# Kernel tuning notes

Measured on AMD Instinct MI355X. Metric: run time of the kernel, lower is better.

## Reference

```python
import jax, jax.numpy as jnp
import numpy as np

# Shapes: [n_boxes, batch, ch, H, W] as produced by Uncropper in the original module.
N_BOXES, BATCH, CH_KQ, CH_V, H, W = 32, 4, 64, 64, 80, 80


def setup_inputs() -> dict:
    key = jax.random.key(0)
    k1, k2, k3 = jax.random.split(key, 3)
    q_big = jax.random.normal(k1, (N_BOXES, BATCH, CH_KQ, H, W), dtype=jnp.float32)
    k_big = jax.random.normal(k2, (N_BOXES, BATCH, CH_KQ, H, W), dtype=jnp.float32)
    v_big = jax.random.normal(k3, (N_BOXES, BATCH, CH_V, H, W), dtype=jnp.float32)
    return {"q_big": q_big, "k_big": k_big, "v_big": v_big}


def reference(q_big, k_big, v_big):
    # Original loop: for i in range(n_boxes):
    #   w = softmax(sum(q_big[i] * k_big, dim=-3, keepdim=True) / sqrt(ch_kq), dim=-5)
    #   delta_big[i] = sum(w * v_big, dim=-5)
    # Vectorized: attention over the box axis, independent per (batch, h, w) pixel.
    scale = 1.0 / np.sqrt(q_big.shape[2]).astype(np.float32)
    # scores[i, j, b, h, w] = <q_big[i, b, :, h, w], k_big[j, b, :, h, w]>
    scores = jnp.einsum('ibchw,jbchw->ijbhw', q_big, k_big) * scale
    w = jax.nn.softmax(scores, axis=1)  # softmax over source box j (dim=-5 in torch)
    delta_big = jnp.einsum('ijbhw,jbchw->ibchw', w, v_big)
    return delta_big
```

## Files before the change

### kernel.cpp

```cpp
#include <hip/hip_runtime.h>


#define NBOX    32
#define NBATCH  4
#define CH      64
#define HW      6400
#define PIX     16
#define NT      512
#define NTILES  (HW / PIX)
#define NUNITS  (NBATCH * NTILES)

typedef __fp16 f16;
typedef f16   f16x2  __attribute__((ext_vector_type(2)));
typedef f16   f16x8  __attribute__((ext_vector_type(8)));
typedef float f32x16 __attribute__((ext_vector_type(16)));

#define SYNC() do { __builtin_amdgcn_sched_barrier(0); __syncthreads(); \
                    __builtin_amdgcn_sched_barrier(0); } while (0)

__device__ __forceinline__ int swz(int L) {
    return L ^ ((((L >> 9) & 3) | (((L >> 13) & 1) << 2)) << 4);
}
__device__ __forceinline__ int swzO(int L) {
    return L ^ ((((L >> 10) & 7) ^ ((L >> 5) & 7)) << 4);
}

#define ZERO16 {0.f,0.f,0.f,0.f,0.f,0.f,0.f,0.f,0.f,0.f,0.f,0.f,0.f,0.f,0.f,0.f}

__global__ __launch_bounds__(NT, 1)
void box_attn_mfma(const float* __restrict__ q, const float* __restrict__ k,
                   const float* __restrict__ v, float* __restrict__ out) {
    __shared__ char sm[65536];
    char* const KF = sm;
    char* const QF = sm + 32768;
    char* const VF = sm;
    char* const OB = sm + 32768;

    const int t    = threadIdx.x;
    const int lane = t & 63;
    const int w    = t >> 6;
    const int h    = lane >> 5;
    const int bid  = blockIdx.x;
    const int unit = (bid & 7) * (NUNITS / 8) + (bid >> 3);
    const int b    = unit / NTILES;
    const int p0   = (unit % NTILES) * PIX;

    auto load_kq = [&](const float* __restrict__ src, int chalf, float4* r) {
#pragma unroll
        for (int rep = 0; rep < 2; ++rep) {
            int u = rep * NT + t;
            int pxq = u & 3, qq = (u >> 2) & 3, kcL = (u >> 4) & 1, box = (u >> 5) & 31;
            int cb = chalf + kcL * 16 + qq * 4;
            const float* g = src + ((size_t)((box * NBATCH + b) * CH + cb)) * HW + p0 + pxq * 4;
            r[rep * 4 + 0] = *(const float4*)(g);
            r[rep * 4 + 1] = *(const float4*)(g + HW);
            r[rep * 4 + 2] = *(const float4*)(g + 2 * HW);
            r[rep * 4 + 3] = *(const float4*)(g + 3 * HW);
        }
    };
    auto write_kq = [&](char* dst, const float4* r) {
#pragma unroll
        for (int rep = 0; rep < 2; ++rep) {
            int u = rep * NT + t;
            int pxq = u & 3, qq = (u >> 2) & 3, kcL = (u >> 4) & 1, box = (u >> 5) & 31;
            int Lb = kcL * 1024 + (box + 32 * (qq & 1)) * 16 + (qq >> 1) * 8;
            const float* f0 = &r[rep * 4 + 0].x;
            const float* f1 = &r[rep * 4 + 1].x;
            const float* f2 = &r[rep * 4 + 2].x;
            const float* f3 = &r[rep * 4 + 3].x;
#pragma unroll
            for (int pi = 0; pi < 4; ++pi) {
                union { f16x2 hh[2]; uint2 u2; } val;
                val.hh[0] = __builtin_amdgcn_cvt_pkrtz(f0[pi], f1[pi]);
                val.hh[1] = __builtin_amdgcn_cvt_pkrtz(f2[pi], f3[pi]);
                *(uint2*)(dst + swz((pxq * 4 + pi) * 2048 + Lb)) = val.u2;
            }
        }
    };
    auto load_v = [&](int coff, float4* r) {
        const size_t JS = (size_t)NBATCH * CH * HW;
#pragma unroll
        for (int rep = 0; rep < 2; ++rep) {
            int u = rep * NT + t;
            int pxq = u & 3, qq = (u >> 2) & 3, jc = (u >> 4) & 1, cL = (u >> 5) & 31;
            const float* g = v + ((size_t)(((jc * 16 + qq * 4) * NBATCH + b) * CH + coff + cL)) * HW
                               + p0 + pxq * 4;
            r[rep * 4 + 0] = *(const float4*)(g);
            r[rep * 4 + 1] = *(const float4*)(g + JS);
            r[rep * 4 + 2] = *(const float4*)(g + 2 * JS);
            r[rep * 4 + 3] = *(const float4*)(g + 3 * JS);
        }
    };
    auto write_v = [&](const float4* r) {
#pragma unroll
        for (int rep = 0; rep < 2; ++rep) {
            int u = rep * NT + t;
            int pxq = u & 3, qq = (u >> 2) & 3, jc = (u >> 4) & 1, cL = (u >> 5) & 31;
            int Lb = jc * 1024 + (cL + 32 * (qq & 1)) * 16 + (qq >> 1) * 8;
            const float* f0 = &r[rep * 4 + 0].x;
            const float* f1 = &r[rep * 4 + 1].x;
            const float* f2 = &r[rep * 4 + 2].x;
            const float* f3 = &r[rep * 4 + 3].x;
#pragma unroll
            for (int pi = 0; pi < 4; ++pi) {
                union { f16x2 hh[2]; uint2 u2; } val;
                val.hh[0] = __builtin_amdgcn_cvt_pkrtz(f0[pi], f1[pi]);
                val.hh[1] = __builtin_amdgcn_cvt_pkrtz(f2[pi], f3[pi]);
                *(uint2*)(VF + swz((pxq * 4 + pi) * 2048 + Lb)) = val.u2;
            }
        }
    };

    auto smax_pack = [&](const f32x16& s, f16x8& fr0, f16x8& fr1) {
        float p[16];
        float m = s[0];
#pragma unroll
        for (int r = 1; r < 16; ++r) m = fmaxf(m, s[r]);
        m = fmaxf(m, __shfl_xor(m, 32, 64));
        float sum = 0.f;
#pragma unroll
        for (int r = 0; r < 16; ++r) { p[r] = __expf((s[r] - m) * 0.125f); sum += p[r]; }
        sum += __shfl_xor(sum, 32, 64);
        float inv = 1.f / sum;
        union { f16x8 v8; f16x2 hh[4]; } u0, u1;
#pragma unroll
        for (int kk = 0; kk < 4; ++kk) {
            u0.hh[kk] = __builtin_amdgcn_cvt_pkrtz(p[2 * kk] * inv,     p[2 * kk + 1] * inv);
            u1.hh[kk] = __builtin_amdgcn_cvt_pkrtz(p[8 + 2 * kk] * inv, p[9 + 2 * kk] * inv);
        }
        fr0 = u0.v8; fr1 = u1.v8;
    };

    f32x16 sA = ZERO16, sB = ZERO16;
    float4 kr[8], qr[8], kr2[8], qr2[8], vr0[8], vr1[8];

    load_kq(k, 0, kr);   load_kq(q, 0, qr);
    load_kq(k, 32, kr2); load_kq(q, 32, qr2);
    load_v(0, vr0);      load_v(32, vr1);

    write_kq(KF, kr);    write_kq(QF, qr);
    SYNC();

#pragma unroll
    for (int kcL = 0; kcL < 2; ++kcL) {
        int LA = kcL * 1024 + lane * 16;
        f16x8 a0 = *(const f16x8*)(KF + swz(w * 2048 + LA));
        f16x8 b0 = *(const f16x8*)(QF + swz(w * 2048 + LA));
        sA = __builtin_amdgcn_mfma_f32_32x32x16_f16(a0, b0, sA, 0, 0, 0);
        f16x8 a1 = *(const f16x8*)(KF + swz((w + 8) * 2048 + LA));
        f16x8 b1 = *(const f16x8*)(QF + swz((w + 8) * 2048 + LA));
        sB = __builtin_amdgcn_mfma_f32_32x32x16_f16(a1, b1, sB, 0, 0, 0);
    }
    SYNC();
    write_kq(KF, kr2); write_kq(QF, qr2);
    SYNC();
#pragma unroll
    for (int kcL = 0; kcL < 2; ++kcL) {
        int LA = kcL * 1024 + lane * 16;
        f16x8 a0 = *(const f16x8*)(KF + swz(w * 2048 + LA));
        f16x8 b0 = *(const f16x8*)(QF + swz(w * 2048 + LA));
        sA = __builtin_amdgcn_mfma_f32_32x32x16_f16(a0, b0, sA, 0, 0, 0);
        f16x8 a1 = *(const f16x8*)(KF + swz((w + 8) * 2048 + LA));
        f16x8 b1 = *(const f16x8*)(QF + swz((w + 8) * 2048 + LA));
        sB = __builtin_amdgcn_mfma_f32_32x32x16_f16(a1, b1, sB, 0, 0, 0);
    }
    SYNC();

    write_v(vr0);
    f16x8 pA0, pA1, pB0, pB1;
    smax_pack(sA, pA0, pA1);
    smax_pack(sB, pB0, pB1);
    SYNC();

    {
        f32x16 oA = ZERO16, oB = ZERO16;
        {
            int LA = lane * 16;
            f16x8 av0 = *(const f16x8*)(VF + swz(w * 2048 + LA));
            oA = __builtin_amdgcn_mfma_f32_32x32x16_f16(av0, pA0, oA, 0, 0, 0);
            f16x8 av1 = *(const f16x8*)(VF + swz((w + 8) * 2048 + LA));
            oB = __builtin_amdgcn_mfma_f32_32x32x16_f16(av1, pB0, oB, 0, 0, 0);
        }
        {
            int LA = 1024 + lane * 16;
            f16x8 av0 = *(const f16x8*)(VF + swz(w * 2048 + LA));
            oA = __builtin_amdgcn_mfma_f32_32x32x16_f16(av0, pA1, oA, 0, 0, 0);
            f16x8 av1 = *(const f16x8*)(VF + swz((w + 8) * 2048 + LA));
            oB = __builtin_amdgcn_mfma_f32_32x32x16_f16(av1, pB1, oB, 0, 0, 0);
        }
        const int i = lane & 31;
#pragma unroll
        for (int r = 0; r < 16; ++r) {
            int cL = (r & 3) + 8 * (r >> 2) + 4 * h;
            *(f16*)(OB + swzO(i * 1024 + cL * 32 + w * 2))       = (f16)oA[r];
            *(f16*)(OB + swzO(i * 1024 + cL * 32 + (w + 8) * 2)) = (f16)oB[r];
        }
        SYNC();

        write_v(vr1);

#pragma unroll
        for (int rep = 0; rep < 2; ++rep) {
            int row = rep * NT + t;
            int oi = row >> 5, cL = row & 31;
            union { uint4 u4; f16x2 hh[4]; } ra, rb;
            ra.u4 = *(const uint4*)(OB + swzO(oi * 1024 + cL * 32));
            rb.u4 = *(const uint4*)(OB + swzO(oi * 1024 + cL * 32 + 16));
            float* op = out + ((size_t)((oi * NBATCH + b) * CH + cL)) * HW + p0;
            float4 s0 = { (float)ra.hh[0][0], (float)ra.hh[0][1], (float)ra.hh[1][0], (float)ra.hh[1][1] };
            float4 s1 = { (float)ra.hh[2][0], (float)ra.hh[2][1], (float)ra.hh[3][0], (float)ra.hh[3][1] };
            float4 s2 = { (float)rb.hh[0][0], (float)rb.hh[0][1], (float)rb.hh[1][0], (float)rb.hh[1][1] };
            float4 s3 = { (float)rb.hh[2][0], (float)rb.hh[2][1], (float)rb.hh[3][0], (float)rb.hh[3][1] };
            *(float4*)(op + 0)  = s0;
            *(float4*)(op + 4)  = s1;
            *(float4*)(op + 8)  = s2;
            *(float4*)(op + 12) = s3;
        }
        SYNC();
    }
    {
        f32x16 oA = ZERO16, oB = ZERO16;
        {
            int LA = lane * 16;
            f16x8 av0 = *(const f16x8*)(VF + swz(w * 2048 + LA));
            oA = __builtin_amdgcn_mfma_f32_32x32x16_f16(av0, pA0, oA, 0, 0, 0);
            f16x8 av1 = *(const f16x8*)(VF + swz((w + 8) * 2048 + LA));
            oB = __builtin_amdgcn_mfma_f32_32x32x16_f16(av1, pB0, oB, 0, 0, 0);
        }
        {
            int LA = 1024 + lane * 16;
            f16x8 av0 = *(const f16x8*)(VF + swz(w * 2048 + LA));
            oA = __builtin_amdgcn_mfma_f32_32x32x16_f16(av0, pA1, oA, 0, 0, 0);
            f16x8 av1 = *(const f16x8*)(VF + swz((w + 8) * 2048 + LA));
            oB = __builtin_amdgcn_mfma_f32_32x32x16_f16(av1, pB1, oB, 0, 0, 0);
        }
        const int i = lane & 31;
#pragma unroll
        for (int r = 0; r < 16; ++r) {
            int cL = (r & 3) + 8 * (r >> 2) + 4 * h;
            *(f16*)(OB + swzO(i * 1024 + cL * 32 + w * 2))       = (f16)oA[r];
            *(f16*)(OB + swzO(i * 1024 + cL * 32 + (w + 8) * 2)) = (f16)oB[r];
        }
        SYNC();

#pragma unroll
        for (int rep = 0; rep < 2; ++rep) {
            int row = rep * NT + t;
            int oi = row >> 5, cL = row & 31;
            union { uint4 u4; f16x2 hh[4]; } ra, rb;
            ra.u4 = *(const uint4*)(OB + swzO(oi * 1024 + cL * 32));
            rb.u4 = *(const uint4*)(OB + swzO(oi * 1024 + cL * 32 + 16));
            float* op = out + ((size_t)((oi * NBATCH + b) * CH + 32 + cL)) * HW + p0;
            float4 s0 = { (float)ra.hh[0][0], (float)ra.hh[0][1], (float)ra.hh[1][0], (float)ra.hh[1][1] };
            float4 s1 = { (float)ra.hh[2][0], (float)ra.hh[2][1], (float)ra.hh[3][0], (float)ra.hh[3][1] };
            float4 s2 = { (float)rb.hh[0][0], (float)rb.hh[0][1], (float)rb.hh[1][0], (float)rb.hh[1][1] };
            float4 s3 = { (float)rb.hh[2][0], (float)rb.hh[2][1], (float)rb.hh[3][0], (float)rb.hh[3][1] };
            *(float4*)(op + 0)  = s0;
            *(float4*)(op + 4)  = s1;
            *(float4*)(op + 8)  = s2;
            *(float4*)(op + 12) = s3;
        }
    }
}

extern "C" void kernel_launch(void* const* d_in, const int* in_sizes, int n_in,
                              void* d_out, int out_size, void* d_ws, size_t ws_size,
                              hipStream_t stream) {
    const float* q = (const float*)d_in[0];
    const float* k = (const float*)d_in[1];
    const float* v = (const float*)d_in[2];
    float* o = (float*)d_out;
    dim3 grid(NUNITS);
    box_attn_mfma<<<grid, NT, 0, stream>>>(q, k, v, o);
}
```

Before: 234.1 us.

## Use inline-asm global loads with explicit vmcnt waits and LDS-only barriers

Global loads now go through inline-asm dwordx4 instructions, and explicit s_waitcnt vmcnt counts let each stage wait only for the loads it needs. Barriers switch to an lgkmcnt-only wait plus s_barrier, so they no longer drain outstanding global loads. The two V register buffers are merged into one reused buffer, with the second V load issued after the first is written, which cuts register pressure and overlaps loads with compute. The vmcnt counts are hand-chosen; if they do not match the actual number of in-flight loads, the kernel will read stale data. Stores made before a barrier are also no longer waited on.

```diff
diff --git a/kernel.cpp b/kernel.cpp
--- a/kernel.cpp
+++ b/kernel.cpp
@@ -15,8 +15,20 @@
 typedef f16   f16x8  __attribute__((ext_vector_type(8)));
 typedef float f32x16 __attribute__((ext_vector_type(16)));
 
-#define SYNC() do { __builtin_amdgcn_sched_barrier(0); __syncthreads(); \
-                    __builtin_amdgcn_sched_barrier(0); } while (0)
+#define SYNCR() do { __builtin_amdgcn_sched_barrier(0); \
+    asm volatile("s_waitcnt lgkmcnt(0)" ::: "memory"); \
+    __builtin_amdgcn_s_barrier(); \
+    __builtin_amdgcn_sched_barrier(0); } while (0)
+
+#define VWAIT(N) do { __builtin_amdgcn_sched_barrier(0); \
+    asm volatile("s_waitcnt vmcnt(" #N ")" ::: "memory"); \
+    __builtin_amdgcn_sched_barrier(0); } while (0)
+
+__device__ __forceinline__ float4 gload(const float* p) {
+    float4 d;
+    asm volatile("global_load_dwordx4 %0, %1, off" : "=v"(d) : "v"(p));
+    return d;
+}
 
 __device__ __forceinline__ int swz(int L) {
     return L ^ ((((L >> 9) & 3) | (((L >> 13) & 1) << 2)) << 4);
@@ -52,10 +64,10 @@
             int pxq = u & 3, qq = (u >> 2) & 3, kcL = (u >> 4) & 1, box = (u >> 5) & 31;
             int cb = chalf + kcL * 16 + qq * 4;
             const float* g = src + ((size_t)((box * NBATCH + b) * CH + cb)) * HW + p0 + pxq * 4;
-            r[rep * 4 + 0] = *(const float4*)(g);
-            r[rep * 4 + 1] = *(const float4*)(g + HW);
-            r[rep * 4 + 2] = *(const float4*)(g + 2 * HW);
-            r[rep * 4 + 3] = *(const float4*)(g + 3 * HW);
+            r[rep * 4 + 0] = gload(g);
+            r[rep * 4 + 1] = gload(g + HW);
+            r[rep * 4 + 2] = gload(g + 2 * HW);
+            r[rep * 4 + 3] = gload(g + 3 * HW);
         }
     };
     auto write_kq = [&](char* dst, const float4* r) {
@@ -85,10 +97,10 @@
             int pxq = u & 3, qq = (u >> 2) & 3, jc = (u >> 4) & 1, cL = (u >> 5) & 31;
             const float* g = v + ((size_t)(((jc * 16 + qq * 4) * NBATCH + b) * CH + coff + cL)) * HW
                                + p0 + pxq * 4;
-            r[rep * 4 + 0] = *(const float4*)(g);
-            r[rep * 4 + 1] = *(const float4*)(g + JS);
-            r[rep * 4 + 2] = *(const float4*)(g + 2 * JS);
-            r[rep * 4 + 3] = *(const float4*)(g + 3 * JS);
+            r[rep * 4 + 0] = gload(g);
+            r[rep * 4 + 1] = gload(g + JS);
+            r[rep * 4 + 2] = gload(g + 2 * JS);
+            r[rep * 4 + 3] = gload(g + 3 * JS);
         }
     };
     auto write_v = [&](const float4* r) {
@@ -131,15 +143,15 @@
         fr0 = u0.v8; fr1 = u1.v8;
     };
 
-    f32x16 sA = ZERO16, sB = ZERO16;
-    float4 kr[8], qr[8], kr2[8], qr2[8], vr0[8], vr1[8];
-
+    float4 kr[8], qr[8], kr2[8], qr2[8], vr[8];
     load_kq(k, 0, kr);   load_kq(q, 0, qr);
     load_kq(k, 32, kr2); load_kq(q, 32, qr2);
-    load_v(0, vr0);      load_v(32, vr1);
-
+
+    VWAIT(16);
     write_kq(KF, kr);    write_kq(QF, qr);
-    SYNC();
+    load_v(0, vr);
+    f32x16 sA = ZERO16, sB = ZERO16;
+    SYNCR();
 
 #pragma unroll
     for (int kcL = 0; kcL < 2; ++kcL) {
@@ -151,9 +163,10 @@
         f16x8 b1 = *(const f16x8*)(QF + swz((w + 8) * 2048 + LA));
         sB = __builtin_amdgcn_mfma_f32_32x32x16_f16(a1, b1, sB, 0, 0, 0);
     }
-    SYNC();
+    SYNCR();
+    VWAIT(8);
     write_kq(KF, kr2); write_kq(QF, qr2);
-    SYNC();
+    SYNCR();
 #pragma unroll
     for (int kcL = 0; kcL < 2; ++kcL) {
         int LA = kcL * 1024 + lane * 16;
@@ -164,13 +177,15 @@
         f16x8 b1 = *(const f16x8*)(QF + swz((w + 8) * 2048 + LA));
         sB = __builtin_amdgcn_mfma_f32_32x32x16_f16(a1, b1, sB, 0, 0, 0);
     }
-    SYNC();
-
-    write_v(vr0);
+    SYNCR();
+
+    VWAIT(0);
+    write_v(vr);
+    load_v(32, vr);
     f16x8 pA0, pA1, pB0, pB1;
     smax_pack(sA, pA0, pA1);
     smax_pack(sB, pB0, pB1);
-    SYNC();
+    SYNCR();
 
     {
         f32x16 oA = ZERO16, oB = ZERO16;
@@ -195,9 +210,10 @@
             *(f16*)(OB + swzO(i * 1024 + cL * 32 + w * 2))       = (f16)oA[r];
             *(f16*)(OB + swzO(i * 1024 + cL * 32 + (w + 8) * 2)) = (f16)oB[r];
         }
-        SYNC();
-
-        write_v(vr1);
+        SYNCR();
+
+        VWAIT(0);
+        write_v(vr);
 
 #pragma unroll
         for (int rep = 0; rep < 2; ++rep) {
@@ -216,7 +232,7 @@
             *(float4*)(op + 8)  = s2;
             *(float4*)(op + 12) = s3;
         }
-        SYNC();
+        SYNCR();
     }
     {
         f32x16 oA = ZERO16, oB = ZERO16;
@@ -241,7 +257,7 @@
             *(f16*)(OB + swzO(i * 1024 + cL * 32 + w * 2))       = (f16)oA[r];
             *(f16*)(OB + swzO(i * 1024 + cL * 32 + (w + 8) * 2)) = (f16)oB[r];
         }
-        SYNC();
+        SYNCR();
 
 #pragma unroll
         for (int rep = 0; rep < 2; ++rep) {
```

Result: faster. 222.0 us (-5.1%).
